# Kernel tuning notes

Measured on AMD Instinct MI355X. Metric: run time of the kernel, lower is better.

## Reference

```python
import jax, jax.numpy as jnp
import numpy as np

CP_SPACING = (4, 4, 4)
SIGMAS = tuple(0.44 * cp for cp in CP_SPACING)


def _gaussian_kernel_3d(sigmas):
    # Faithful to DeepReg layer_util.gaussian_filter_3d
    ks = [int(np.ceil(s * 3) + np.mod(np.ceil(s * 3) + 1, 2)) for s in sigmas]
    grid = np.stack(np.meshgrid(*[np.arange(k) for k in ks], indexing="ij"), axis=0)  # [3,k,k,k]
    mean = ((np.asarray(ks, np.float64) - 1.0) / 2.0).reshape(-1, 1, 1, 1)
    var = (np.asarray(sigmas, np.float64) ** 2.0).reshape(-1, 1, 1, 1)
    norm = 1.0 / (np.sqrt(2.0 * np.pi) ** 3 + np.prod(sigmas))  # as in DeepReg source
    kernel = norm * np.exp(-np.sum((grid - mean) ** 2.0 / (2.0 * var), axis=0))
    kernel = kernel / np.sum(kernel)  # sums to 1
    return kernel.astype(np.float32)  # [k,k,k]


def setup_inputs() -> dict:
    key = jax.random.key(0)
    image = jax.random.normal(key, (4, 160, 160, 160, 3), dtype=jnp.float32)  # DDF volume, 3 channels
    kernel = jnp.asarray(_gaussian_kernel_3d(SIGMAS))  # deterministic [7,7,7] Gaussian buffer
    return {"image": image, "kernel": kernel}


def reference(image, kernel):
    b, d1, d2, d3, c = image.shape
    # DeepReg's [k,k,k,3,3] diagonal kernel == depthwise blur per channel.
    kdw = jnp.tile(kernel[..., None, None], (1, 1, 1, 1, c))  # [k,k,k,1,C]
    blurred = jax.lax.conv_general_dilated(
        image, kdw,
        window_strides=(1, 1, 1),
        padding="SAME",
        dimension_numbers=("NDHWC", "DHWIO", "NDHWC"),
        feature_group_count=c,
    )
    # output control-point grid: ceil(dim / cp_spacing) + 3
    size = tuple(int(np.ceil(v / cp)) + 3 for v, cp in zip((d1, d2, d3), CP_SPACING))
    # tf.image.resize bilinear (TF2) uses half-pixel centers == jax.image.resize 'linear'
    out = jax.image.resize(blurred, (b,) + size + (c,), method="linear")
    return out
```

## Files before the change

### kernel.cpp

```cpp
#include <hip/hip_runtime.h>
#include <hip/hip_fp16.h>

#define NB 4
#define NI 160
#define NO 43
#define NC 3
#define KS 7
#define KPAD 3
#define MT 16
#define CH 8
#define CH1 4
#define P1B 128
#define NP 22

#define ROWF (NI * NC)
#define PROW 132
#define PROW4 (PROW / 4)
#define LROW 484
#define SLICE (NO * NO * NC)

#define A1H_BYTES ((size_t)NB * NI * NI * PROW * 2)
#define A2H_BYTES ((size_t)NB * NI * NO * PROW * 2)
#define P2P_THREADS ((size_t)NB * NI * NP * PROW4)
#define P3_THREADS ((size_t)NB * NO * NO * PROW4)

struct __align__(16) Tables {
    float w1[NO][MT];
    float wp[NP][24][2];
    int   o1hp[NP][24];
    int   o0h[NO][MT];
    int   j3[NO];
    int   jlo[NO];
};

constexpr double ctaylor(double r) {
    double s = 1.0, term = 1.0;
    for (int n = 1; n <= 13; ++n) { term *= r / (double)n; s += term; }
    return s;
}
constexpr double cexp_neg(double x) {
    double y = -x;
    int k = (int)(y * 16.0);
    double r = y - (double)k / 16.0;
    double e16 = ctaylor(1.0 / 16.0);
    double p = 1.0;
    for (int i = 0; i < k; ++i) p *= e16;
    return 1.0 / (p * ctaylor(r));
}
constexpr int cceil(double x)  { int c = (int)x; return ((double)c < x) ? c + 1 : c; }
constexpr int cfloor(double x) { int f = (int)x; return ((double)f > x) ? f - 1 : f; }
constexpr double cabsd(double x) { return x < 0 ? -x : x; }

constexpr double comp_w(int j, double sf, int ilo, int ihi, const double* g) {
    if (j >= NI || j < 0) return 0.0;
    double cw = 0.0;
    for (int t = 0; t < KS; ++t) {
        int i = j + KPAD - t;
        if (i >= ilo && i <= ihi) {
            double w = 1.0 - cabsd(sf - (double)i) * (43.0 / 160.0);
            if (w > 0.0) cw += g[t] * w;
        }
    }
    return cw;
}

struct Band { double sf; int ilo; int ihi; double wsum; };
constexpr Band bandof(int o) {
    const double inv_scale = 160.0 / 43.0;
    double sf = ((double)o + 0.5) * inv_scale - 0.5;
    int ilo = cceil(sf - inv_scale);  if (ilo < 0) ilo = 0;
    int ihi = cfloor(sf + inv_scale); if (ihi > NI - 1) ihi = NI - 1;
    double wsum = 0.0;
    for (int i = ilo; i <= ihi; ++i) {
        double w = 1.0 - cabsd(sf - (double)i) * (43.0 / 160.0);
        if (w > 0.0) wsum += w;
    }
    return {sf, ilo, ihi, wsum};
}

constexpr Tables make_tables() {
    Tables T{};
    double g[KS] = {};
    double gs = 0.0;
    const double sig = 0.44 * 4.0;
    for (int i = 0; i < KS; ++i) {
        double d = (double)i - 3.0;
        g[i] = cexp_neg(-(d * d) / (2.0 * sig * sig));
        gs += g[i];
    }
    for (int i = 0; i < KS; ++i) g[i] /= gs;

    for (int o = 0; o < NO; ++o) {
        Band B = bandof(o);
        int jlo = B.ilo - KPAD; if (jlo < 0) jlo = 0;
        T.j3[o] = jlo & ~3;
        T.jlo[o] = jlo;
        for (int k = 0; k < MT; ++k) {
            int j = jlo + k;
            T.w1[o][k] = (float)(comp_w(j, B.sf, B.ilo, B.ihi, g) / B.wsum);
            int jc = (j < NI) ? j : (NI - 1);
            T.o0h[o][k] = jc * (NO * PROW * 2);
        }
    }
    for (int p = 0; p < NP; ++p) {
        int oA = 2 * p, oB = 2 * p + 1;
        Band BA = bandof(oA);
        int jp = T.j3[oA];
        for (int k = 0; k < 24; ++k) {
            T.wp[p][k][0] = (float)(comp_w(jp + k, BA.sf, BA.ilo, BA.ihi, g) / BA.wsum);
            if (oB < NO) {
                Band BB = bandof(oB);
                T.wp[p][k][1] = (float)(comp_w(jp + k, BB.sf, BB.ilo, BB.ihi, g) / BB.wsum);
            } else {
                T.wp[p][k][1] = 0.0f;
            }
            int jc = (jp + k < NI) ? (jp + k) : (NI - 1);
            T.o1hp[p][k] = jc * (PROW * 2);
        }
    }
    return T;
}

__constant__ Tables dT = make_tables();

struct __align__(8) h4 { __half2 lo, hi; };
union h2u { __half2 h; unsigned int u; };

__global__ __launch_bounds__(P1B) void k_p1(
        const float* __restrict__ img, __half* __restrict__ A1h) {
    __shared__ __align__(16) float rows[CH1 * LROW + 64];
    int t = threadIdx.x;
    int blk = blockIdx.x;

    const int p = t % NP, row = t / NP;
    const bool has = (t < NP * CH1);

    float4 wq0, wq1, wq2, wq3, wq4, wq5, wq6, wq7, wq8, wq9, wq10, wq11;
    int jp = 0;
    if (has) {
        jp = dT.j3[2 * p];
        const float4* wpp = (const float4*)dT.wp[p];
        wq0 = wpp[0];  wq1 = wpp[1];  wq2 = wpp[2];  wq3 = wpp[3];
        wq4 = wpp[4];  wq5 = wpp[5];  wq6 = wpp[6];  wq7 = wpp[7];
        wq8 = wpp[8];  wq9 = wpp[9];  wq10 = wpp[10]; wq11 = wpp[11];
    }

    const float4* src = (const float4*)(img + (size_t)blk * (CH1 * ROWF));
    for (int g = t; g < CH1 * ROWF / 4; g += P1B) {
        int r = g / 120, m = g % 120;
        *(float4*)(rows + r * LROW + 4 * m) = src[g];
    }
    if (t < 16) rows[(t >> 2) * LROW + ROWF + (t & 3)] = 0.f;
    if (t >= 16 && t < 80) rows[CH1 * LROW + (t - 16)] = 0.f;
    __syncthreads();

    if (has) {
        const float4* dp = (const float4*)(rows + row * LROW + 3 * jp);
        float a0 = 0.f, a1 = 0.f, a2 = 0.f;
        float b0 = 0.f, b1 = 0.f, b2 = 0.f;
#define STEP(M, WQA, WQB) {                                                    \
            float4 v0 = dp[3*(M)], v1 = dp[3*(M)+1], v2 = dp[3*(M)+2];         \
            a0 += WQA.x * v0.x; a1 += WQA.x * v0.y; a2 += WQA.x * v0.z;        \
            b0 += WQA.y * v0.x; b1 += WQA.y * v0.y; b2 += WQA.y * v0.z;        \
            a0 += WQA.z * v0.w; a1 += WQA.z * v1.x; a2 += WQA.z * v1.y;        \
            b0 += WQA.w * v0.w; b1 += WQA.w * v1.x; b2 += WQA.w * v1.y;        \
            a0 += WQB.x * v1.z; a1 += WQB.x * v1.w; a2 += WQB.x * v2.x;        \
            b0 += WQB.y * v1.z; b1 += WQB.y * v1.w; b2 += WQB.y * v2.x;        \
            a0 += WQB.z * v2.y; a1 += WQB.z * v2.z; a2 += WQB.z * v2.w;        \
            b0 += WQB.w * v2.y; b1 += WQB.w * v2.z; b2 += WQB.w * v2.w;        \
        }
        STEP(0, wq0, wq1)  STEP(1, wq2, wq3)  STEP(2, wq4, wq5)
        STEP(3, wq6, wq7)  STEP(4, wq8, wq9)  STEP(5, wq10, wq11)
#undef STEP
        h2u c0, c1, c2;
        c0.h = __floats2half2_rn(a0, a1);
        c1.h = __floats2half2_rn(a2, b0);
        c2.h = __floats2half2_rn(b1, b2);
        unsigned int* dstu = (unsigned int*)A1h;
        size_t baseu = ((size_t)blk * CH1 + row) * (PROW / 2) + 3 * p;
        dstu[baseu] = c0.u; dstu[baseu + 1] = c1.u; dstu[baseu + 2] = c2.u;
    }
}

__device__ __forceinline__ int xcd_swz(int wg, int nwg) {
    int q = nwg >> 3, r = nwg & 7;
    int x = wg & 7, i = wg >> 3;
    return (x < r ? x * (q + 1) : r * (q + 1) + (x - r) * q) + i;
}

__global__ __launch_bounds__(256) void k_p2(
        const __half* __restrict__ A1h, __half* __restrict__ A2h) {
    int blk = xcd_swz(blockIdx.x, gridDim.x);
    size_t idx = (size_t)blk * 256 + threadIdx.x;
    if (idx >= P2P_THREADS) return;
    int ii = (int)idx;
    int col4 = ii % PROW4;
    int p    = (ii / PROW4) % NP;
    int slab = ii / (PROW4 * NP);
    const char* base = (const char*)A1h + ((size_t)slab * NI * PROW + col4 * 4) * 2;
    const float4* wpp = (const float4*)dT.wp[p];
    const int4*   ot  = (const int4*)dT.o1hp[p];
    float4 wq0 = wpp[0], wq1 = wpp[1], wq2 = wpp[2],  wq3 = wpp[3];
    float4 wq4 = wpp[4], wq5 = wpp[5], wq6 = wpp[6],  wq7 = wpp[7];
    float4 wq8 = wpp[8], wq9 = wpp[9], wq10 = wpp[10], wq11 = wpp[11];
    int4 t0 = ot[0], t1 = ot[1], t2 = ot[2], t3 = ot[3], t4 = ot[4], t5 = ot[5];
    float4 a = {0.f,0.f,0.f,0.f}, b = a;
#define TP(J, WA, WB) { h4 v = *(const h4*)(base + (unsigned)(J));             \
        float2 f0 = __half22float2(v.lo), f1 = __half22float2(v.hi);           \
        a.x += (WA) * f0.x; a.y += (WA) * f0.y;                                \
        a.z += (WA) * f1.x; a.w += (WA) * f1.y;                                \
        b.x += (WB) * f0.x; b.y += (WB) * f0.y;                                \
        b.z += (WB) * f1.x; b.w += (WB) * f1.y; }
    TP(t0.x, wq0.x, wq0.y)  TP(t0.y, wq0.z, wq0.w)
    TP(t0.z, wq1.x, wq1.y)  TP(t0.w, wq1.z, wq1.w)
    TP(t1.x, wq2.x, wq2.y)  TP(t1.y, wq2.z, wq2.w)
    TP(t1.z, wq3.x, wq3.y)  TP(t1.w, wq3.z, wq3.w)
    TP(t2.x, wq4.x, wq4.y)  TP(t2.y, wq4.z, wq4.w)
    TP(t2.z, wq5.x, wq5.y)  TP(t2.w, wq5.z, wq5.w)
    TP(t3.x, wq6.x, wq6.y)  TP(t3.y, wq6.z, wq6.w)
    TP(t3.z, wq7.x, wq7.y)  TP(t3.w, wq7.z, wq7.w)
    TP(t4.x, wq8.x, wq8.y)  TP(t4.y, wq8.z, wq8.w)
    TP(t4.z, wq9.x, wq9.y)  TP(t4.w, wq9.z, wq9.w)
    TP(t5.x, wq10.x, wq10.y) TP(t5.y, wq10.z, wq10.w)
    TP(t5.z, wq11.x, wq11.y) TP(t5.w, wq11.z, wq11.w)
#undef TP
    h4* A2h4 = (h4*)A2h;
    size_t rbase = ((size_t)slab * NO + 2 * p) * PROW4 + col4;
    h4 ra; ra.lo = __floats2half2_rn(a.x, a.y); ra.hi = __floats2half2_rn(a.z, a.w);
    A2h4[rbase] = ra;
    if (2 * p + 1 < NO) {
        h4 rb; rb.lo = __floats2half2_rn(b.x, b.y); rb.hi = __floats2half2_rn(b.z, b.w);
        A2h4[rbase + PROW4] = rb;
    }
}

__global__ __launch_bounds__(256) void k_p3(
        const __half* __restrict__ A2h, float* __restrict__ out) {
    int blk = xcd_swz(blockIdx.x, gridDim.x);
    size_t idx = (size_t)blk * 256 + threadIdx.x;
    if (idx >= P3_THREADS) return;
    int ii = (int)idx;
    int col4 = ii % PROW4;
    int o2   = (ii / PROW4) % NO;
    int o1   = (ii / (PROW4 * NO)) % NO;
    int b    = ii / (PROW4 * NO * NO);
    const char* base = (const char*)A2h +
        (((size_t)b * NI * NO + o2) * PROW + col4 * 4) * 2;
    const float4* wv = (const float4*)dT.w1[o1];
    const int4*   ov = (const int4*)dT.o0h[o1];
    float4 w0 = wv[0], w1v = wv[1], w2 = wv[2], w3 = wv[3];
    int4   j0 = ov[0], j1 = ov[1], j2 = ov[2], j3 = ov[3];
    float4 a = {0.f, 0.f, 0.f, 0.f};
#define TAP4H(J, W) { h4 v = *(const h4*)(base + (unsigned)(J));               \
                      float2 f0 = __half22float2(v.lo);                        \
                      float2 f1 = __half22float2(v.hi);                        \
                      a.x += (W) * f0.x; a.y += (W) * f0.y;                    \
                      a.z += (W) * f1.x; a.w += (W) * f1.y; }
    TAP4H(j0.x, w0.x) TAP4H(j0.y, w0.y) TAP4H(j0.z, w0.z) TAP4H(j0.w, w0.w)
    TAP4H(j1.x, w1v.x) TAP4H(j1.y, w1v.y) TAP4H(j1.z, w1v.z) TAP4H(j1.w, w1v.w)
    TAP4H(j2.x, w2.x) TAP4H(j2.y, w2.y) TAP4H(j2.z, w2.z) TAP4H(j2.w, w2.w)
    TAP4H(j3.x, w3.x) TAP4H(j3.y, w3.y) TAP4H(j3.z, w3.z) TAP4H(j3.w, w3.w)
#undef TAP4H
    int tile = (b * NO + o1) * NO + o2;
    float* ob = out + (size_t)tile * (NO * NC) + col4 * 4;
    int col = col4 * 4;
    float av[4] = {a.x, a.y, a.z, a.w};
    #pragma unroll
    for (int e = 0; e < 4; ++e)
        if (col + e < NO * NC) ob[e] = av[e];
}

__global__ __launch_bounds__(256) void k_passA(
        const float* __restrict__ img, float* __restrict__ S) {
    __shared__ float rows[CH * NI * NC];
    __shared__ float T[CH * NO * NC];
    __shared__ float acc[NO * NO * NC];
    __shared__ float w2[NO * MT];
    __shared__ int   s2[NO];
    int t = threadIdx.x;
    int blk = blockIdx.x;
    const float* src = img + (size_t)blk * (NI * NI * NC);
    for (int k = t; k < NO * MT; k += 256) w2[k] = ((const float*)dT.w1)[k];
    for (int k = t; k < NO; k += 256) s2[k] = dT.jlo[k];
    for (int k = t; k < NO * NO * NC; k += 256) acc[k] = 0.f;
    __syncthreads();
    for (int chunk = 0; chunk < NI / CH; ++chunk) {
        const float4* csrc = (const float4*)(src + (size_t)chunk * CH * NI * NC);
        for (int k = t; k < CH * NI * NC / 4; k += 256)
            ((float4*)rows)[k] = csrc[k];
        __syncthreads();
        for (int task = t; task < CH * NO; task += 256) {
            int ch = task / NO, o3 = task % NO;
            int st = s2[o3];
            const float* rp = rows + ch * NI * NC;
            float a0 = 0.f, a1 = 0.f, a2 = 0.f;
            #pragma unroll
            for (int k = 0; k < MT; ++k) {
                int j = st + k; j = (j < NI) ? j : (NI - 1);
                float w = w2[o3 * MT + k];
                a0 += w * rp[j * 3 + 0];
                a1 += w * rp[j * 3 + 1];
                a2 += w * rp[j * 3 + 2];
            }
            T[task * NC + 0] = a0;
            T[task * NC + 1] = a1;
            T[task * NC + 2] = a2;
        }
        __syncthreads();
        int i2base = chunk * CH;
        for (int task = t; task < NO * NO; task += 256) {
            int o2 = task / NO, o3 = task % NO;
            int st = s2[o2];
            int k0 = i2base - st;        k0 = (k0 > 0) ? k0 : 0;
            int k1 = i2base + CH - st;   k1 = (k1 < MT) ? k1 : MT;
            if (k1 > k0) {
                float a0 = 0.f, a1 = 0.f, a2 = 0.f;
                for (int k = k0; k < k1; ++k) {
                    float w = w2[o2 * MT + k];
                    int ch = st + k - i2base;
                    a0 += w * T[(ch * NO + o3) * NC + 0];
                    a1 += w * T[(ch * NO + o3) * NC + 1];
                    a2 += w * T[(ch * NO + o3) * NC + 2];
                }
                acc[task * NC + 0] += a0;
                acc[task * NC + 1] += a1;
                acc[task * NC + 2] += a2;
            }
        }
        __syncthreads();
    }
    float* Sp = S + (size_t)blk * (NO * NO * NC);
    for (int k = t; k < NO * NO * NC; k += 256) Sp[k] = acc[k];
}

__global__ __launch_bounds__(256) void k_passB(
        const float* __restrict__ S, float* __restrict__ out) {
    int blk = blockIdx.x;
    int b = blk / NO, o1 = blk % NO;
    __shared__ float w1s[MT];
    __shared__ int s1v;
    if (threadIdx.x < MT) w1s[threadIdx.x] = dT.w1[o1][threadIdx.x];
    if (threadIdx.x == 0) s1v = dT.jlo[o1];
    __syncthreads();
    const float* Sb = S + (size_t)b * NI * (NO * NO * NC);
    float* ob = out + (size_t)blk * (NO * NO * NC);
    int st = s1v;
    for (int e = threadIdx.x; e < NO * NO * NC; e += 256) {
        float a = 0.f;
        #pragma unroll
        for (int k = 0; k < MT; ++k) {
            int i1 = st + k; i1 = (i1 < NI) ? i1 : (NI - 1);
            a += w1s[k] * Sb[(size_t)i1 * (NO * NO * NC) + e];
        }
        ob[e] = a;
    }
}

extern "C" void kernel_launch(void* const* d_in, const int* in_sizes, int n_in,
                              void* d_out, int out_size, void* d_ws, size_t ws_size,
                              hipStream_t stream) {
    (void)in_sizes; (void)n_in; (void)out_size;
    const float* img = (const float*)d_in[0];
    float* out = (float*)d_out;
    char* ws = (char*)d_ws;

    if (ws_size >= A1H_BYTES + A2H_BYTES) {
        __half* A1h = (__half*)ws;
        __half* A2h = (__half*)(ws + A1H_BYTES);
        k_p1<<<NB * NI * (NI / CH1), P1B, 0, stream>>>(img, A1h);
        int p2b = (int)((P2P_THREADS + 255) / 256);
        k_p2<<<p2b, 256, 0, stream>>>(A1h, A2h);
        int p3b = (int)((P3_THREADS + 255) / 256);
        k_p3<<<p3b, 256, 0, stream>>>(A2h, out);
    } else {
        float* S = (float*)ws;
        k_passA<<<NB * NI, 256, 0, stream>>>(img, S);
        k_passB<<<NB * NO, 256, 0, stream>>>(S, out);
    }
}
```

Baseline: 67.47 us.

## Load pass-1 input rows directly from global memory into registers, dropping LDS staging

The first pass no longer stages four input rows per block in shared memory behind a barrier. Each thread now reads its own 18 float4 window straight from global memory into registers, with a per-output-pair count table handling the row-end tail. The launch becomes a flat 256-thread grid with no idle lanes. This removes the LDS round trip and the sync, but neighbouring threads read overlapping windows, so it relies on the cache to absorb the redundant global loads and uses more registers.

```diff
diff --git a/kernel.cpp b/kernel.cpp
--- a/kernel.cpp
+++ b/kernel.cpp
@@ -9,18 +9,16 @@
 #define KPAD 3
 #define MT 16
 #define CH 8
-#define CH1 4
-#define P1B 128
 #define NP 22
 
 #define ROWF (NI * NC)
 #define PROW 132
 #define PROW4 (PROW / 4)
-#define LROW 484
 #define SLICE (NO * NO * NC)
 
 #define A1H_BYTES ((size_t)NB * NI * NI * PROW * 2)
 #define A2H_BYTES ((size_t)NB * NI * NO * PROW * 2)
+#define P1_THREADS ((size_t)NB * NI * NI * NP)
 #define P2P_THREADS ((size_t)NB * NI * NP * PROW4)
 #define P3_THREADS ((size_t)NB * NO * NO * PROW4)
 
@@ -31,6 +29,7 @@
     int   o0h[NO][MT];
     int   j3[NO];
     int   jlo[NO];
+    int   nq[NP];
 };
 
 constexpr double ctaylor(double r) {
@@ -117,6 +116,9 @@
             int jc = (jp + k < NI) ? (jp + k) : (NI - 1);
             T.o1hp[p][k] = jc * (PROW * 2);
         }
+        int q0 = (3 * jp) / 4;
+        int nq = 120 - q0; if (nq > 18) nq = 18;
+        T.nq[p] = nq;
     }
     return T;
 }
@@ -126,60 +128,51 @@
 struct __align__(8) h4 { __half2 lo, hi; };
 union h2u { __half2 h; unsigned int u; };
 
-__global__ __launch_bounds__(P1B) void k_p1(
+__global__ __launch_bounds__(256) void k_p1(
         const float* __restrict__ img, __half* __restrict__ A1h) {
-    __shared__ __align__(16) float rows[CH1 * LROW + 64];
-    int t = threadIdx.x;
-    int blk = blockIdx.x;
-
-    const int p = t % NP, row = t / NP;
-    const bool has = (t < NP * CH1);
-
-    float4 wq0, wq1, wq2, wq3, wq4, wq5, wq6, wq7, wq8, wq9, wq10, wq11;
-    int jp = 0;
-    if (has) {
-        jp = dT.j3[2 * p];
-        const float4* wpp = (const float4*)dT.wp[p];
-        wq0 = wpp[0];  wq1 = wpp[1];  wq2 = wpp[2];  wq3 = wpp[3];
-        wq4 = wpp[4];  wq5 = wpp[5];  wq6 = wpp[6];  wq7 = wpp[7];
-        wq8 = wpp[8];  wq9 = wpp[9];  wq10 = wpp[10]; wq11 = wpp[11];
-    }
-
-    const float4* src = (const float4*)(img + (size_t)blk * (CH1 * ROWF));
-    for (int g = t; g < CH1 * ROWF / 4; g += P1B) {
-        int r = g / 120, m = g % 120;
-        *(float4*)(rows + r * LROW + 4 * m) = src[g];
-    }
-    if (t < 16) rows[(t >> 2) * LROW + ROWF + (t & 3)] = 0.f;
-    if (t >= 16 && t < 80) rows[CH1 * LROW + (t - 16)] = 0.f;
-    __syncthreads();
-
-    if (has) {
-        const float4* dp = (const float4*)(rows + row * LROW + 3 * jp);
-        float a0 = 0.f, a1 = 0.f, a2 = 0.f;
-        float b0 = 0.f, b1 = 0.f, b2 = 0.f;
+    size_t idx = (size_t)blockIdx.x * 256 + threadIdx.x;
+    if (idx >= P1_THREADS) return;
+    int ii = (int)idx;
+    int p  = ii % NP;
+    int gr = ii / NP;
+    int jp = dT.j3[2 * p];
+    int q0 = (3 * jp) >> 2;
+    int nq = dT.nq[p];
+
+    const float4* wpp = (const float4*)dT.wp[p];
+    float4 wq0 = wpp[0],  wq1 = wpp[1],  wq2 = wpp[2],  wq3 = wpp[3];
+    float4 wq4 = wpp[4],  wq5 = wpp[5],  wq6 = wpp[6],  wq7 = wpp[7];
+    float4 wq8 = wpp[8],  wq9 = wpp[9],  wq10 = wpp[10], wq11 = wpp[11];
+
+    const float4* rp = (const float4*)(img + (size_t)gr * ROWF) + q0;
+    const float4 z4 = {0.f, 0.f, 0.f, 0.f};
+    float4 r[18];
+    #pragma unroll
+    for (int q = 0; q < 18; ++q) r[q] = (q < nq) ? rp[q] : z4;
+
+    float a0 = 0.f, a1 = 0.f, a2 = 0.f;
+    float b0 = 0.f, b1 = 0.f, b2 = 0.f;
 #define STEP(M, WQA, WQB) {                                                    \
-            float4 v0 = dp[3*(M)], v1 = dp[3*(M)+1], v2 = dp[3*(M)+2];         \
-            a0 += WQA.x * v0.x; a1 += WQA.x * v0.y; a2 += WQA.x * v0.z;        \
-            b0 += WQA.y * v0.x; b1 += WQA.y * v0.y; b2 += WQA.y * v0.z;        \
-            a0 += WQA.z * v0.w; a1 += WQA.z * v1.x; a2 += WQA.z * v1.y;        \
-            b0 += WQA.w * v0.w; b1 += WQA.w * v1.x; b2 += WQA.w * v1.y;        \
-            a0 += WQB.x * v1.z; a1 += WQB.x * v1.w; a2 += WQB.x * v2.x;        \
-            b0 += WQB.y * v1.z; b1 += WQB.y * v1.w; b2 += WQB.y * v2.x;        \
-            a0 += WQB.z * v2.y; a1 += WQB.z * v2.z; a2 += WQB.z * v2.w;        \
-            b0 += WQB.w * v2.y; b1 += WQB.w * v2.z; b2 += WQB.w * v2.w;        \
-        }
-        STEP(0, wq0, wq1)  STEP(1, wq2, wq3)  STEP(2, wq4, wq5)
-        STEP(3, wq6, wq7)  STEP(4, wq8, wq9)  STEP(5, wq10, wq11)
+        float4 v0 = r[3*(M)], v1 = r[3*(M)+1], v2 = r[3*(M)+2];                \
+        a0 += WQA.x * v0.x; a1 += WQA.x * v0.y; a2 += WQA.x * v0.z;            \
+        b0 += WQA.y * v0.x; b1 += WQA.y * v0.y; b2 += WQA.y * v0.z;            \
+        a0 += WQA.z * v0.w; a1 += WQA.z * v1.x; a2 += WQA.z * v1.y;            \
+        b0 += WQA.w * v0.w; b1 += WQA.w * v1.x; b2 += WQA.w * v1.y;            \
+        a0 += WQB.x * v1.z; a1 += WQB.x * v1.w; a2 += WQB.x * v2.x;            \
+        b0 += WQB.y * v1.z; b1 += WQB.y * v1.w; b2 += WQB.y * v2.x;            \
+        a0 += WQB.z * v2.y; a1 += WQB.z * v2.z; a2 += WQB.z * v2.w;            \
+        b0 += WQB.w * v2.y; b1 += WQB.w * v2.z; b2 += WQB.w * v2.w;            \
+    }
+    STEP(0, wq0, wq1)  STEP(1, wq2, wq3)  STEP(2, wq4, wq5)
+    STEP(3, wq6, wq7)  STEP(4, wq8, wq9)  STEP(5, wq10, wq11)
 #undef STEP
-        h2u c0, c1, c2;
-        c0.h = __floats2half2_rn(a0, a1);
-        c1.h = __floats2half2_rn(a2, b0);
-        c2.h = __floats2half2_rn(b1, b2);
-        unsigned int* dstu = (unsigned int*)A1h;
-        size_t baseu = ((size_t)blk * CH1 + row) * (PROW / 2) + 3 * p;
-        dstu[baseu] = c0.u; dstu[baseu + 1] = c1.u; dstu[baseu + 2] = c2.u;
-    }
+    h2u c0, c1, c2;
+    c0.h = __floats2half2_rn(a0, a1);
+    c1.h = __floats2half2_rn(a2, b0);
+    c2.h = __floats2half2_rn(b1, b2);
+    unsigned int* dstu = (unsigned int*)A1h;
+    size_t baseu = (size_t)gr * (PROW / 2) + 3 * p;
+    dstu[baseu] = c0.u; dstu[baseu + 1] = c1.u; dstu[baseu + 2] = c2.u;
 }
 
 __device__ __forceinline__ int xcd_swz(int wg, int nwg) {
@@ -367,7 +360,8 @@
     if (ws_size >= A1H_BYTES + A2H_BYTES) {
         __half* A1h = (__half*)ws;
         __half* A2h = (__half*)(ws + A1H_BYTES);
-        k_p1<<<NB * NI * (NI / CH1), P1B, 0, stream>>>(img, A1h);
+        int p1b = (int)((P1_THREADS + 255) / 256);
+        k_p1<<<p1b, 256, 0, stream>>>(img, A1h);
         int p2b = (int)((P2P_THREADS + 255) / 256);
         k_p2<<<p2b, 256, 0, stream>>>(A1h, A2h);
         int p3b = (int)((P3_THREADS + 255) / 256);
```

Result: slower. 198.1 us (+193.7%).
